# Kernel tuning notes

Measured on AMD Instinct MI355X. Metric: run time of the kernel, lower is better.

Reference implementation:

```python
import jax, jax.numpy as jnp
import numpy as np

B = 1024        # batch of clips
MAX_LEN = 14    # temporal length, pinned by spatial_shapes=[[max_len,1]]
D_MODEL = 1024
N_HEADS = 16
N_POINTS = 4
H_SP, W_SP = MAX_LEN, 1  # level-0 spatial shape (H, W)


def setup_inputs() -> dict:
    key = jax.random.key(0)
    ks = jax.random.split(key, 12)
    s = 0.02
    lin = lambda k, i, o: (jax.random.normal(k, (i, o), jnp.float32) * s)
    vec = lambda k, o: (jax.random.normal(k, (o,), jnp.float32) * s)
    return {
        "x": jax.random.normal(ks[0], (B, MAX_LEN, D_MODEL), jnp.float32),
        "W_value": lin(ks[1], D_MODEL, D_MODEL), "b_value": vec(ks[2], D_MODEL),
        "W_off": lin(ks[3], D_MODEL, N_HEADS * N_POINTS * 2), "b_off": vec(ks[4], N_HEADS * N_POINTS * 2),
        "W_attn": lin(ks[5], D_MODEL, N_HEADS * N_POINTS), "b_attn": vec(ks[6], N_HEADS * N_POINTS),
        "W_out": lin(ks[7], D_MODEL, D_MODEL), "b_out": vec(ks[8], D_MODEL),
        "W_proj": lin(ks[9], D_MODEL, D_MODEL), "b_proj": vec(ks[10], D_MODEL),
    }


def _msdeform(x, W_value, b_value, W_off, b_off, W_attn, b_attn, W_out, b_out):
    Bq, T, D = x.shape
    heads, P = N_HEADS, N_POINTS
    hd = D // heads
    # value projection -> [B, heads, N=H*W, hd]
    value = (x @ W_value + b_value).reshape(Bq, T, heads, hd).transpose(0, 2, 1, 3)
    # sampling offsets [B,T,heads,P,2] and softmax attention weights [B,T,heads,P]
    off = (x @ W_off + b_off).reshape(Bq, T, heads, P, 2)
    aw = jax.nn.softmax((x @ W_attn + b_attn).reshape(Bq, T, heads, P), axis=-1)
    # reference points: x-coord = linspace(0,1,T), y-coord = 0
    ref = jnp.linspace(0.0, 1.0, T, dtype=x.dtype)
    ref_pts = jnp.stack([ref, jnp.zeros_like(ref)], axis=-1)  # [T,2]
    norm = jnp.array([W_SP, H_SP], dtype=x.dtype)  # offset_normalizer = (W, H)
    locs = ref_pts[None, :, None, None, :] + off / norm  # [B,T,heads,P,2] in [0,1] coords
    # grid_sample bilinear, align_corners=False, padding_mode='zeros':
    # pixel coord = loc * size - 0.5
    ix = locs[..., 0] * W_SP - 0.5
    iy = locs[..., 1] * H_SP - 0.5
    x0 = jnp.floor(ix); y0 = jnp.floor(iy)
    fx = ix - x0; fy = iy - y0
    x0i = x0.astype(jnp.int32); y0i = y0.astype(jnp.int32)
    out = jnp.zeros((Bq, heads, T * P, hd), x.dtype)
    corners = ((0, 0, (1 - fx) * (1 - fy)), (1, 0, fx * (1 - fy)),
               (0, 1, (1 - fx) * fy), (1, 1, fx * fy))
    for dx, dy, w in corners:
        xx = x0i + dx; yy = y0i + dy
        valid = ((xx >= 0) & (xx < W_SP) & (yy >= 0) & (yy < H_SP)).astype(x.dtype)
        idx = jnp.clip(yy, 0, H_SP - 1) * W_SP + jnp.clip(xx, 0, W_SP - 1)  # [B,T,heads,P]
        idx_t = idx.transpose(0, 2, 1, 3).reshape(Bq, heads, T * P)
        v = jnp.take_along_axis(value, idx_t[..., None], axis=2)  # [B,heads,T*P,hd]
        wt = (w * valid).transpose(0, 2, 1, 3).reshape(Bq, heads, T * P)
        out = out + v * wt[..., None]
    out = out.reshape(Bq, heads, T, P, hd)
    attn = jnp.einsum('bhqpd,bqhp->bqhd', out, aw).reshape(Bq, T, D)
    return attn @ W_out + b_out


def reference(x, W_value, b_value, W_off, b_off, W_attn, b_attn, W_out, b_out, W_proj, b_proj):
    y = _msdeform(x, W_value, b_value, W_off, b_off, W_attn, b_attn, W_out, b_out)
    return y @ W_proj + b_proj
```

## Files before the change

kernel.cpp:

```cpp
#include <hip/hip_runtime.h>
#include <hip/hip_bf16.h>

using bf16 = __hip_bfloat16;
typedef __attribute__((ext_vector_type(8))) short bf16x8;
typedef __attribute__((ext_vector_type(4))) float f32x4;

#define NB   1024
#define TT   14
#define DM   1024
#define ROWS (NB*TT)
#define NCAT 1280

__device__ __forceinline__ unsigned short f2b(float f) {
  union { bf16 h; unsigned short u; } cv; cv.h = __float2bfloat16(f); return cv.u;
}

__device__ __forceinline__ void gload16(const bf16* g, bf16* l) {
  __builtin_amdgcn_global_load_lds((const __attribute__((address_space(1))) void*)g,
                                   (__attribute__((address_space(3))) void*)l, 16, 0, 0);
}

__global__ __launch_bounds__(256) void k_prep_all(
    const float* __restrict__ x_in,
    const float* __restrict__ Wv, const float* __restrict__ Wo,
    const float* __restrict__ Wa, const float* __restrict__ Wproj,
    const float* __restrict__ Wout,
    const float* __restrict__ bv, const float* __restrict__ bo,
    const float* __restrict__ ba, const float* __restrict__ b_out,
    const float* __restrict__ b_proj,
    bf16* __restrict__ x_bf,
    bf16* __restrict__ wcat_t, bf16* __restrict__ wproj_t,
    bf16* __restrict__ wout_b, float* __restrict__ bcat,
    float* __restrict__ bcomb) {
  __shared__ float t[32][33];
  const int x = blockIdx.x, y = blockIdx.y;
  const int lx = threadIdx.x & 31, ly = threadIdx.x >> 5;
  if (y < 72) {
    const float* src; bf16* dst; int base, width;
    if (y < 40) {
      dst = wcat_t;
      int n0 = y * 32;
      if (n0 < 1024)      { src = Wv; base = 0;    width = 1024; }
      else if (n0 < 1152) { src = Wo; base = 1024; width = 128;  }
      else if (n0 < 1216) { src = Wa; base = 1152; width = 64;   }
      else                { src = nullptr; base = 0; width = 1;  }
      int k0 = x * 32, n0b = n0;
#pragma unroll
      for (int r = 0; r < 32; r += 8)
        t[ly + r][lx] = src ? src[(size_t)(k0 + ly + r) * width + (n0b - base + lx)] : 0.0f;
      __syncthreads();
#pragma unroll
      for (int r = 0; r < 32; r += 8)
        dst[(size_t)(n0b + ly + r) * 1024 + (k0 + lx)] = __float2bfloat16(t[lx][ly + r]);
    } else {
      int n0 = (y - 40) * 32, k0 = x * 32;
#pragma unroll
      for (int r = 0; r < 32; r += 8)
        t[ly + r][lx] = Wproj[(size_t)(k0 + ly + r) * 1024 + (n0 + lx)];
      __syncthreads();
#pragma unroll
      for (int r = 0; r < 32; r += 8)
        wproj_t[(size_t)(n0 + ly + r) * 1024 + (k0 + lx)] = __float2bfloat16(t[lx][ly + r]);
    }
  } else if (y < 80) {
    int i0 = ((y - 72) * 32 + x) * 1024 + threadIdx.x;
#pragma unroll
    for (int r = 0; r < 4; ++r) {
      int i = i0 + r * 256;
      float4 v = reinterpret_cast<const float4*>(Wout)[i];
      ushort4 o;
      o.x = f2b(v.x); o.y = f2b(v.y); o.z = f2b(v.z); o.w = f2b(v.w);
      reinterpret_cast<ushort4*>(wout_b)[i] = o;
    }
  } else if (y == 80) {
    if (x < 5) {
      int i = x * 256 + threadIdx.x;
      if (i < NCAT) {
        float v = 0.0f;
        if (i < 1024) v = bv[i];
        else if (i < 1152) v = bo[i - 1024];
        else if (i < 1216) v = ba[i - 1152];
        bcat[i] = v;
      }
    } else if (x < 21) {
      __shared__ float part[4][64];
      int j0 = (x - 5) * 64;
      int jl = threadIdx.x & 63, ip = threadIdx.x >> 6;
      int j = j0 + jl;
      float acc = 0.0f;
      int i0 = ip * 256;
      for (int i = i0; i < i0 + 256; ++i)
        acc = fmaf(b_out[i], Wproj[(size_t)i * 1024 + j], acc);
      part[ip][jl] = acc;
      __syncthreads();
      if (threadIdx.x < 64) {
        int jj = j0 + threadIdx.x;
        bcomb[jj] = part[0][threadIdx.x] + part[1][threadIdx.x] +
                    part[2][threadIdx.x] + part[3][threadIdx.x] + b_proj[jj];
      }
    }
  } else {
    int id = (y - 81) * 32 + x;
    int i0 = id * 2048 + threadIdx.x;
#pragma unroll
    for (int r = 0; r < 8; ++r) {
      int i = i0 + r * 256;
      float4 v = reinterpret_cast<const float4*>(x_in)[i];
      ushort4 o;
      o.x = f2b(v.x); o.y = f2b(v.y); o.z = f2b(v.z); o.w = f2b(v.w);
      reinterpret_cast<ushort4*>(x_bf)[i] = o;
    }
  }
}

template<int OUT1, int OUT2>
__global__ __launch_bounds__(256, 3) void k_gemm_dual(
    const bf16* __restrict__ A1, const bf16* __restrict__ B1,
    void* __restrict__ C1v, const float* __restrict__ bias1,
    int N1, int K1, int lda1, int ldb1, int nx1, int nwg1,
    const bf16* __restrict__ A2, const bf16* __restrict__ B2,
    void* __restrict__ C2v, const float* __restrict__ bias2,
    int N2, int K2, int lda2, int ldb2, int nx2) {
  constexpr int ASZ = 4096, BSZ = 4096;
  __shared__ bf16 As[3 * ASZ];
  __shared__ bf16 Bs[3 * BSZ];

  const int tid  = threadIdx.x;
  const int wave = tid >> 6, lane = tid & 63;

  const bf16 *A, *Bt; void* Cv; const float* bias;
  int N, K, lda, ldb, bx, by; bool ob;
  if ((int)blockIdx.x < nwg1) {
    int bid = blockIdx.x;
    int q = nwg1 >> 3, r = nwg1 & 7;
    int xcd = bid & 7, li = bid >> 3;
    bid = (xcd < r ? xcd * (q + 1) : r * (q + 1) + (xcd - r) * q) + li;
    A = A1; Bt = B1; Cv = C1v; bias = bias1;
    N = N1; K = K1; lda = lda1; ldb = ldb1;
    bx = bid % nx1; by = bid / nx1; ob = (OUT1 != 0);
  } else {
    int bid = blockIdx.x - nwg1;
    A = A2; Bt = B2; Cv = C2v; bias = bias2;
    N = N2; K = K2; lda = lda2; ldb = ldb2;
    bx = bid % nx2; by = bid / nx2; ob = (OUT2 != 0);
  }
  const int row0 = by * 128, col0 = bx * 128;
  const int wr = (wave >> 1) * 64, wc = (wave & 1) * 64;
  f32x4 acc[4][4] = {};

  const int sr  = tid >> 2;
  const int scb = (tid & 3) ^ ((sr + (sr >> 2)) & 3);
  const bf16* Ab = A  + (size_t)(row0 + sr) * lda + scb * 8;
  const bf16* Bb = Bt + (size_t)(col0 + sr) * ldb + scb * 8;

  const int fr = lane & 15, g = lane >> 4;
  int aoff[4], boff[4];
#pragma unroll
  for (int mi = 0; mi < 4; ++mi) {
    int row = wr + mi * 16 + fr, h = row >> 6, lr = row & 63;
    aoff[mi] = h * 2048 + (lr * 4 + (g ^ ((lr + (lr >> 2)) & 3))) * 8;
  }
#pragma unroll
  for (int ni = 0; ni < 4; ++ni) {
    int row = wc + ni * 16 + fr, h = row >> 6, lr = row & 63;
    boff[ni] = h * 2048 + (lr * 4 + (g ^ ((lr + (lr >> 2)) & 3))) * 8;
  }

  auto STAGE = [&](int s, int kk) {
    const int ko = kk * 32;
#pragma unroll
    for (int j = 0; j < 2; ++j)
      gload16(Ab + (size_t)j * 64 * lda + ko, As + s * ASZ + j * 2048 + tid * 8);
#pragma unroll
    for (int j = 0; j < 2; ++j)
      gload16(Bb + (size_t)j * 64 * ldb + ko, Bs + s * BSZ + j * 2048 + tid * 8);
  };
  auto COMPUTE = [&](int s) {
    const bf16* as = As + s * ASZ;
    const bf16* bs = Bs + s * BSZ;
    bf16x8 af[4], bfm[4];
#pragma unroll
    for (int mi = 0; mi < 4; ++mi) af[mi] = *(const bf16x8*)(as + aoff[mi]);
#pragma unroll
    for (int ni = 0; ni < 4; ++ni) bfm[ni] = *(const bf16x8*)(bs + boff[ni]);
    __builtin_amdgcn_s_setprio(1);
#pragma unroll
    for (int mi = 0; mi < 4; ++mi)
#pragma unroll
      for (int ni = 0; ni < 4; ++ni)
        acc[mi][ni] = __builtin_amdgcn_mfma_f32_16x16x32_bf16(bfm[ni], af[mi], acc[mi][ni], 0, 0, 0);
    __builtin_amdgcn_s_setprio(0);
  };

  const int nk = K >> 5;
  STAGE(0, 0);
  STAGE(1, 1);
  int cur = 0;
  for (int i = 0; i < nk; ++i) {
    if (i < nk - 1) asm volatile("s_waitcnt vmcnt(4)" ::: "memory");
    else            asm volatile("s_waitcnt vmcnt(0)" ::: "memory");
    __builtin_amdgcn_s_barrier();
    asm volatile("" ::: "memory");
    if (i + 2 < nk) {
      int s2 = cur + 2; if (s2 >= 3) s2 -= 3;
      STAGE(s2, i + 2);
    }
    COMPUTE(cur);
    if (++cur == 3) cur = 0;
  }

  const int fq = g * 4;
#pragma unroll
  for (int mi = 0; mi < 4; ++mi) {
    int gr = row0 + wr + mi * 16 + fr;
#pragma unroll
    for (int ni = 0; ni < 4; ++ni) {
      int gc = col0 + wc + ni * 16 + fq;
      float b0 = 0, b1 = 0, b2 = 0, b3 = 0;
      if (bias) {
        float4 bv = *reinterpret_cast<const float4*>(bias + gc);
        b0 = bv.x; b1 = bv.y; b2 = bv.z; b3 = bv.w;
      }
      float v0 = acc[mi][ni][0] + b0, v1 = acc[mi][ni][1] + b1;
      float v2 = acc[mi][ni][2] + b2, v3 = acc[mi][ni][3] + b3;
      if (ob) {
        ushort4 u; u.x = f2b(v0); u.y = f2b(v1); u.z = f2b(v2); u.w = f2b(v3);
        *reinterpret_cast<ushort4*>((bf16*)Cv + (size_t)gr * N + gc) = u;
      } else {
        float4 o; o.x = v0; o.y = v1; o.z = v2; o.w = v3;
        *reinterpret_cast<float4*>((float*)Cv + (size_t)gr * N + gc) = o;
      }
    }
  }
}

__global__ __launch_bounds__(256) void k_sample(const bf16* __restrict__ C1,
                                                bf16* __restrict__ y) {
  const int wave = threadIdx.x >> 6, lane = threadIdx.x & 63;
  const int row = blockIdx.x * 4 + wave;
  const int b = row / TT, t = row - b * TT;
  const bf16* r1 = C1 + (size_t)row * NCAT;

  float offx, offy;
  {
    ushort2 u = *reinterpret_cast<const ushort2*>(r1 + 1024 + lane * 2);
    offx = __uint_as_float(((unsigned)u.x) << 16);
    offy = __uint_as_float(((unsigned)u.y) << 16);
  }
  float logit;
  {
    unsigned short u = reinterpret_cast<const unsigned short*>(r1)[1152 + lane];
    logit = __uint_as_float(((unsigned)u) << 16);
  }
  float m = fmaxf(logit, __shfl_xor(logit, 1));
  m = fmaxf(m, __shfl_xor(m, 2));
  float e = __expf(logit - m);
  float s = e + __shfl_xor(e, 1);
  s = s + __shfl_xor(s, 2);
  float aw = e / s;

  const float refx = (float)t * (1.0f / 13.0f);
  float ix = refx + offx - 0.5f;
  float xf = floorf(ix);
  float fx = ix - xf;
  float wx = (xf == 0.0f) ? (1.0f - fx) : ((xf == -1.0f) ? fx : 0.0f);

  float iy = offy - 0.5f;
  float yf = floorf(iy);
  float fy = iy - yf;
  int y0 = (int)yf, y1 = y0 + 1;
  float w0 = (y0 >= 0 && y0 < TT) ? (1.0f - fy) : 0.0f;
  float w1 = (y1 >= 0 && y1 < TT) ? fy : 0.0f;
  int i0 = max(0, min(TT - 1, y0));
  int i1 = max(0, min(TT - 1, y1));
  float cw0 = aw * wx * w0;
  float cw1 = aw * wx * w1;

  const bf16* vb = C1 + (size_t)(b * TT) * NCAT;
  float acc[16];
#pragma unroll
  for (int h = 0; h < 16; ++h) acc[h] = 0.0f;
#pragma unroll
  for (int j = 0; j < 64; ++j) {
    float c0 = __shfl(cw0, j);
    float c1 = __shfl(cw1, j);
    int a0 = __shfl(i0, j);
    int a1 = __shfl(i1, j);
    const int hh = j >> 2;
    float v0 = __bfloat162float(vb[(size_t)a0 * NCAT + hh * 64 + lane]);
    float v1 = __bfloat162float(vb[(size_t)a1 * NCAT + hh * 64 + lane]);
    acc[hh] = fmaf(c0, v0, fmaf(c1, v1, acc[hh]));
  }
#pragma unroll
  for (int h = 0; h < 16; ++h)
    y[(size_t)row * DM + h * 64 + lane] = __float2bfloat16(acc[h]);
}

extern "C" void kernel_launch(void* const* d_in, const int* in_sizes, int n_in,
                              void* d_out, int out_size, void* d_ws, size_t ws_size,
                              hipStream_t stream) {
  (void)in_sizes; (void)n_in; (void)out_size; (void)ws_size;
  const float* x       = (const float*)d_in[0];
  const float* W_value = (const float*)d_in[1];
  const float* b_value = (const float*)d_in[2];
  const float* W_off   = (const float*)d_in[3];
  const float* b_off   = (const float*)d_in[4];
  const float* W_attn  = (const float*)d_in[5];
  const float* b_attn  = (const float*)d_in[6];
  const float* W_out   = (const float*)d_in[7];
  const float* b_out   = (const float*)d_in[8];
  const float* W_proj  = (const float*)d_in[9];
  const float* b_proj  = (const float*)d_in[10];

  char* ws = (char*)d_ws;
  bf16*  x_bf    = (bf16*)(ws);
  bf16*  y_bf    = x_bf;
  bf16*  C1      = (bf16*)(ws + 29360128);
  bf16*  Wcat_t  = (bf16*)(ws + 66060288);
  float* bcat    = (float*)(ws + 68681728);
  bf16*  Wout_b  = (bf16*)(ws + 68686848);
  bf16*  Wproj_t = (bf16*)(ws + 70784000);
  bf16*  Wc_t    = (bf16*)(ws + 72881152);
  float* bcomb   = (float*)(ws + 74978304);

  k_prep_all<<<dim3(32, 137), 256, 0, stream>>>(
      x, W_value, W_off, W_attn, W_proj, W_out,
      b_value, b_off, b_attn, b_out, b_proj,
      x_bf, Wcat_t, Wproj_t, Wout_b, bcat, bcomb);

  k_gemm_dual<1, 1><<<1120 + 64, 256, 0, stream>>>(
      x_bf, Wcat_t, C1, bcat, NCAT, DM, DM, DM, NCAT / 128, 1120,
      Wproj_t, Wout_b, Wc_t, nullptr, 1024, 1024, 1024, 1024, 8);

  k_sample<<<ROWS / 4, 256, 0, stream>>>(C1, y_bf);

  k_gemm_dual<0, 0><<<896, 256, 0, stream>>>(
      y_bf, Wc_t, (float*)d_out, bcomb, DM, DM, DM, DM, DM / 128, 896,
      y_bf, Wc_t, (float*)d_out, bcomb, DM, DM, DM, DM, DM / 128);
}
```

Before: 182.9 us.

## Enlarge GEMM tile to 256x128 with eight waves and simpler LDS swizzle

The dual GEMM kernel now uses 512-thread workgroups that each compute a 256x128 output tile with eight waves, so every B tile loaded into LDS is shared by twice as many rows. This halves the workgroup count and cuts redundant B-operand traffic. The LDS swizzle changes to a plain XOR on the low row bits with a contiguous 32-element row layout. Risks are higher LDS use per block, lower occupancy, fewer workgroups for the 304... CUs, and possible new bank conflicts from the simpler swizzle. The secondary GEMM in the dual launch (W_proj x W_out, 8x8 tiles of 128) now covers 256-row tiles with 32 blocks, so it stays consistent.

```diff
diff --git a/kernel.cpp b/kernel.cpp
--- a/kernel.cpp
+++ b/kernel.cpp
@@ -114,19 +114,18 @@
 }
 
 template<int OUT1, int OUT2>
-__global__ __launch_bounds__(256, 3) void k_gemm_dual(
+__global__ __launch_bounds__(512, 4) void k_gemm2(
     const bf16* __restrict__ A1, const bf16* __restrict__ B1,
     void* __restrict__ C1v, const float* __restrict__ bias1,
     int N1, int K1, int lda1, int ldb1, int nx1, int nwg1,
     const bf16* __restrict__ A2, const bf16* __restrict__ B2,
     void* __restrict__ C2v, const float* __restrict__ bias2,
     int N2, int K2, int lda2, int ldb2, int nx2) {
-  constexpr int ASZ = 4096, BSZ = 4096;
-  __shared__ bf16 As[3 * ASZ];
-  __shared__ bf16 Bs[3 * BSZ];
-
-  const int tid  = threadIdx.x;
-  const int wave = tid >> 6, lane = tid & 63;
+  __shared__ bf16 As[3 * 8192];
+  __shared__ bf16 Bs[3 * 4096];
+
+  const int tid = threadIdx.x, w = tid >> 6, l = tid & 63;
+  const int wm = w >> 1, wn = w & 1;
 
   const bf16 *A, *Bt; void* Cv; const float* bias;
   int N, K, lda, ldb, bx, by; bool ob;
@@ -144,45 +143,38 @@
     N = N2; K = K2; lda = lda2; ldb = ldb2;
     bx = bid % nx2; by = bid / nx2; ob = (OUT2 != 0);
   }
-  const int row0 = by * 128, col0 = bx * 128;
-  const int wr = (wave >> 1) * 64, wc = (wave & 1) * 64;
+  const int row0 = by * 256, col0 = bx * 128;
   f32x4 acc[4][4] = {};
 
-  const int sr  = tid >> 2;
-  const int scb = (tid & 3) ^ ((sr + (sr >> 2)) & 3);
-  const bf16* Ab = A  + (size_t)(row0 + sr) * lda + scb * 8;
-  const bf16* Bb = Bt + (size_t)(col0 + sr) * ldb + scb * 8;
-
-  const int fr = lane & 15, g = lane >> 4;
+  const int sr = tid >> 2;
+  const int sc = ((tid & 3) ^ (sr & 3)) * 8;
+  const bf16* Ab0 = A  + (size_t)(row0 + sr) * lda + sc;
+  const bf16* Ab1 = Ab0 + (size_t)128 * lda;
+  const bf16* Bb  = Bt + (size_t)(col0 + sr) * ldb + sc;
+
+  const int fr = l & 15, g = l >> 4;
+  const int fs = (g ^ (fr & 3)) * 8;
   int aoff[4], boff[4];
 #pragma unroll
-  for (int mi = 0; mi < 4; ++mi) {
-    int row = wr + mi * 16 + fr, h = row >> 6, lr = row & 63;
-    aoff[mi] = h * 2048 + (lr * 4 + (g ^ ((lr + (lr >> 2)) & 3))) * 8;
-  }
-#pragma unroll
-  for (int ni = 0; ni < 4; ++ni) {
-    int row = wc + ni * 16 + fr, h = row >> 6, lr = row & 63;
-    boff[ni] = h * 2048 + (lr * 4 + (g ^ ((lr + (lr >> 2)) & 3))) * 8;
-  }
-
-  auto STAGE = [&](int s, int kk) {
-    const int ko = kk * 32;
-#pragma unroll
-    for (int j = 0; j < 2; ++j)
-      gload16(Ab + (size_t)j * 64 * lda + ko, As + s * ASZ + j * 2048 + tid * 8);
-#pragma unroll
-    for (int j = 0; j < 2; ++j)
-      gload16(Bb + (size_t)j * 64 * ldb + ko, Bs + s * BSZ + j * 2048 + tid * 8);
+  for (int i = 0; i < 4; ++i) {
+    aoff[i] = (wm * 64 + i * 16 + fr) * 32 + fs;
+    boff[i] = (wn * 64 + i * 16 + fr) * 32 + fs;
+  }
+
+  auto STAGE = [&](int s, int kt) {
+    const int ko = kt * 32;
+    gload16(Ab0 + ko, As + s * 8192 + tid * 8);
+    gload16(Ab1 + ko, As + s * 8192 + 4096 + tid * 8);
+    gload16(Bb  + ko, Bs + s * 4096 + tid * 8);
   };
   auto COMPUTE = [&](int s) {
-    const bf16* as = As + s * ASZ;
-    const bf16* bs = Bs + s * BSZ;
+    const bf16* as = As + s * 8192;
+    const bf16* bs = Bs + s * 4096;
     bf16x8 af[4], bfm[4];
 #pragma unroll
-    for (int mi = 0; mi < 4; ++mi) af[mi] = *(const bf16x8*)(as + aoff[mi]);
-#pragma unroll
-    for (int ni = 0; ni < 4; ++ni) bfm[ni] = *(const bf16x8*)(bs + boff[ni]);
+    for (int i = 0; i < 4; ++i) af[i]  = *(const bf16x8*)(as + aoff[i]);
+#pragma unroll
+    for (int i = 0; i < 4; ++i) bfm[i] = *(const bf16x8*)(bs + boff[i]);
     __builtin_amdgcn_s_setprio(1);
 #pragma unroll
     for (int mi = 0; mi < 4; ++mi)
@@ -196,26 +188,25 @@
   STAGE(0, 0);
   STAGE(1, 1);
   int cur = 0;
-  for (int i = 0; i < nk; ++i) {
-    if (i < nk - 1) asm volatile("s_waitcnt vmcnt(4)" ::: "memory");
+  for (int t = 0; t < nk; ++t) {
+    if (t < nk - 1) asm volatile("s_waitcnt vmcnt(3)" ::: "memory");
     else            asm volatile("s_waitcnt vmcnt(0)" ::: "memory");
     __builtin_amdgcn_s_barrier();
     asm volatile("" ::: "memory");
-    if (i + 2 < nk) {
+    if (t + 2 < nk) {
       int s2 = cur + 2; if (s2 >= 3) s2 -= 3;
-      STAGE(s2, i + 2);
+      STAGE(s2, t + 2);
     }
     COMPUTE(cur);
     if (++cur == 3) cur = 0;
   }
 
-  const int fq = g * 4;
 #pragma unroll
   for (int mi = 0; mi < 4; ++mi) {
-    int gr = row0 + wr + mi * 16 + fr;
+    int gr = row0 + wm * 64 + mi * 16 + fr;
 #pragma unroll
     for (int ni = 0; ni < 4; ++ni) {
-      int gc = col0 + wc + ni * 16 + fq;
+      int gc = col0 + wn * 64 + ni * 16 + g * 4;
       float b0 = 0, b1 = 0, b2 = 0, b3 = 0;
       if (bias) {
         float4 bv = *reinterpret_cast<const float4*>(bias + gc);
@@ -328,13 +319,13 @@
       b_value, b_off, b_attn, b_out, b_proj,
       x_bf, Wcat_t, Wproj_t, Wout_b, bcat, bcomb);
 
-  k_gemm_dual<1, 1><<<1120 + 64, 256, 0, stream>>>(
-      x_bf, Wcat_t, C1, bcat, NCAT, DM, DM, DM, NCAT / 128, 1120,
+  k_gemm2<1, 1><<<560 + 32, 512, 0, stream>>>(
+      x_bf, Wcat_t, C1, bcat, NCAT, DM, DM, DM, NCAT / 128, 560,
       Wproj_t, Wout_b, Wc_t, nullptr, 1024, 1024, 1024, 1024, 8);
 
   k_sample<<<ROWS / 4, 256, 0, stream>>>(C1, y_bf);
 
-  k_gemm_dual<0, 0><<<896, 256, 0, stream>>>(
-      y_bf, Wc_t, (float*)d_out, bcomb, DM, DM, DM, DM, DM / 128, 896,
+  k_gemm2<0, 0><<<448, 512, 0, stream>>>(
+      y_bf, Wc_t, (float*)d_out, bcomb, DM, DM, DM, DM, DM / 128, 448,
       y_bf, Wc_t, (float*)d_out, bcomb, DM, DM, DM, DM, DM / 128);
 }
```

After: 176.6 us. 1.04x faster.
